# Optimization experiments

Measured on AMD Instinct MI355X. Metric: run time of the kernel, lower is better.

## Reference

```python
import jax, jax.numpy as jnp
import numpy as np

BATCH = 1024
INPUT_DIM = 4096
HIDDEN_DIM = 4096
N_BLOCKS = 8
BLOCK_SIZE = HIDDEN_DIM // N_BLOCKS          # 512
IN_BLOCK_SIZE = INPUT_DIM // N_BLOCKS        # 512


def setup_inputs() -> dict:
    key = jax.random.key(0)
    ks = jax.random.split(key, 6)
    scale = 1.0 / np.sqrt(BLOCK_SIZE)  # torch GRUCell init: U(-1/sqrt(hidden), 1/sqrt(hidden))
    return {
        "x": jax.random.normal(ks[0], (BATCH, INPUT_DIM), dtype=jnp.float32),
        "h": jax.random.normal(ks[1], (BATCH, HIDDEN_DIM), dtype=jnp.float32),
        "W_ih": jax.random.normal(ks[2], (N_BLOCKS, 3 * BLOCK_SIZE, IN_BLOCK_SIZE), dtype=jnp.float32) * scale,
        "W_hh": jax.random.normal(ks[3], (N_BLOCKS, 3 * BLOCK_SIZE, BLOCK_SIZE), dtype=jnp.float32) * scale,
        "b_ih": jax.random.normal(ks[4], (N_BLOCKS, 3 * BLOCK_SIZE), dtype=jnp.float32) * scale,
        "b_hh": jax.random.normal(ks[5], (N_BLOCKS, 3 * BLOCK_SIZE), dtype=jnp.float32) * scale,
    }


def reference(x, h, W_ih, W_hh, b_ih, b_hh):
    B = x.shape[0]
    n, g3, ibs = W_ih.shape           # n_blocks, 3*block_size, input_block_size
    bs = W_hh.shape[2]                # block_size
    xb = x.reshape(B, n, ibs)         # (B, n_blocks, input_block_size)
    hb = h.reshape(B, n, bs)          # (B, n_blocks, block_size)
    # Block-diagonal GEMM: one grouped matmul over all blocks at once.
    gi = jnp.einsum('bni,ngi->bng', xb, W_ih) + b_ih   # (B, n, 3*bs)
    gh = jnp.einsum('bnh,ngh->bng', hb, W_hh) + b_hh   # (B, n, 3*bs)
    i_r, i_z, i_n = jnp.split(gi, 3, axis=-1)
    h_r, h_z, h_n = jnp.split(gh, 3, axis=-1)
    r = jax.nn.sigmoid(i_r + h_r)                      # reset gate
    z = jax.nn.sigmoid(i_z + h_z)                      # update gate
    n_gate = jnp.tanh(i_n + r * h_n)                   # candidate state
    new_h = n_gate + z * (hb - n_gate)                 # torch GRUCell: h' = (1-z)*n + z*h
    return new_h.reshape(B, n * bs)
```

## Files before the change

### kernel.cpp

```cpp
#include <hip/hip_runtime.h>
#include <hip/hip_bf16.h>
#include <stdint.h>

#define G1CAST(p) ((const __attribute__((address_space(1))) void*)(p))
#define L3CAST(p) ((__attribute__((address_space(3))) void*)(p))

typedef short bf16x8 __attribute__((ext_vector_type(8)));
typedef float f32x16 __attribute__((ext_vector_type(16)));

static __device__ __forceinline__ short f2bf(float f) {
    __hip_bfloat16 b = __float2bfloat16(f);
    return __builtin_bit_cast(short, b);
}

__global__ __launch_bounds__(256) void wconv_kernel(const float* __restrict__ Wih,
                                                    const float* __restrict__ Whh,
                                                    short* __restrict__ Wstep) {
    const int b = blockIdx.x;
    const int vb = (b & 7) * 768 + (b >> 3);
    const int gid = vb * 256 + threadIdx.x;
    const int lane = gid & 63;
    int t1 = gid >> 6;
    const int g = t1 % 3;  t1 /= 3;
    const int wn = t1 & 1; t1 >>= 1;
    const int s = t1 & 63; t1 >>= 6;
    const int jt = t1 & 7;
    const int nblk = t1 >> 3;
    const int j = jt * 64 + wn * 32 + (lane & 31);
    const int kk = s * 16 + (lane >> 5) * 8;
    const float* src = (kk < 512)
        ? Wih + ((int64_t)nblk * 786432 + (int64_t)(g * 512 + j) * 512 + kk)
        : Whh + ((int64_t)nblk * 786432 + (int64_t)(g * 512 + j) * 512 + (kk - 512));
    const float4 a = ((const float4*)src)[0];
    const float4 bq = ((const float4*)src)[1];
    bf16x8 o;
    o[0] = f2bf(a.x); o[1] = f2bf(a.y); o[2] = f2bf(a.z); o[3] = f2bf(a.w);
    o[4] = f2bf(bq.x); o[5] = f2bf(bq.y); o[6] = f2bf(bq.z); o[7] = f2bf(bq.w);
    *(bf16x8*)(Wstep + (size_t)gid * 8) = o;
}

__global__ __launch_bounds__(256) void aconv_kernel(const float* __restrict__ x,
                                                    const float* __restrict__ h,
                                                    short* __restrict__ Afrag) {
    const int b = blockIdx.x;
    const int n = b & 7;
    const int inner = b >> 3;
    const int rb = inner >> 4;
    const int u = inner & 15;
    const int tid = threadIdx.x;
    const int lane = tid & 63;
    const int s = u * 4 + (tid >> 6);
    const int row = rb * 32 + (lane & 31);
    const int kk = s * 16 + (lane >> 5) * 8;
    const float* src = (kk < 512)
        ? x + ((size_t)row * 4096 + n * 512 + kk)
        : h + ((size_t)row * 4096 + n * 512 + (kk - 512));
    const float4 a = ((const float4*)src)[0];
    const float4 bq = ((const float4*)src)[1];
    bf16x8 o;
    o[0] = f2bf(a.x); o[1] = f2bf(a.y); o[2] = f2bf(a.z); o[3] = f2bf(a.w);
    o[4] = f2bf(bq.x); o[5] = f2bf(bq.y); o[6] = f2bf(bq.z); o[7] = f2bf(bq.w);
    const size_t dst = ((((size_t)(rb * 8 + n) * 64 + s) * 64) + lane) * 8;
    *(bf16x8*)(Afrag + dst) = o;
}

__global__ __launch_bounds__(256, 2) void gru_kernel(
    const float* __restrict__ hst,
    const short* __restrict__ Wstep, const short* __restrict__ Afrag,
    const float* __restrict__ b_ih, const float* __restrict__ b_hh,
    float* __restrict__ out)
{
    __shared__ char ldsB[6][8192];

    const int tid = threadIdx.x;
    const int nblk = blockIdx.x & 7;
    const int rr_ = blockIdx.x >> 3;
    const int bt = rr_ >> 3;
    const int jt = rr_ & 7;
    const int brow0 = bt * 128;

    const int lane = tid & 63;
    const int wave = tid >> 6;
    const int wm = wave >> 1;
    const int wn = wave & 1;
    const int l31 = lane & 31;
    const int k8 = lane >> 5;

    const int rb0 = (brow0 + wm * 64) >> 5;
    const char* ab0 = (const char*)Afrag + ((size_t)(rb0 * 8 + nblk) << 16) + (size_t)lane * 16;
    const char* ab1 = ab0 + (8 << 16);

    const int d0 = wave * 2048;
    const int ssrc0 = (d0 >= 6144) ? d0 - 6144 : d0;
    const int ssrc1 = (d0 + 1024 >= 6144) ? d0 + 1024 - 6144 : d0 + 1024;
    const char* wstep0 = (const char*)Wstep + (size_t)((nblk * 8 + jt) * 64) * 6144
                       + (size_t)lane * 16;
    const int boff = (wn * 3) * 1024 + lane * 16;

    f32x16 acc_r[2] = {};
    f32x16 acc_z[2] = {};
    f32x16 acc_nx[2] = {};
    f32x16 acc_nh[2] = {};

    bf16x8 a0P, a1P, a0Q, a1Q, a0R, a1R, a0S, a1S;

#define LDA(T, s_v)                                                        \
    {                                                                      \
        const int sc = (s_v) > 63 ? 63 : (s_v);                            \
        a0##T = *(const bf16x8*)(ab0 + (size_t)sc * 1024);                 \
        a1##T = *(const bf16x8*)(ab1 + (size_t)sc * 1024);                 \
    }

    auto stageB = [&](int s, int slot) {
        const int sc = s > 63 ? 63 : s;
        const char* src = wstep0 + (size_t)sc * 6144;
        char* dst = (char*)&ldsB[slot][0] + d0;
        __builtin_amdgcn_global_load_lds(G1CAST(src + ssrc0), L3CAST(dst), 16, 0, 0);
        __builtin_amdgcn_global_load_lds(G1CAST(src + ssrc1), L3CAST(dst + 1024), 16, 0, 0);
    };

#define ITER(C, L, accN)                                                            \
    {                                                                               \
        __builtin_amdgcn_s_barrier();                                               \
        __builtin_amdgcn_sched_barrier(0);                                          \
        stageB(s_ + 5, wslot);                                                      \
        LDA(L, s_ + 3)                                                              \
        __builtin_amdgcn_sched_barrier(0);                                          \
        asm volatile("s_waitcnt vmcnt(12)" ::: "memory");                           \
        __builtin_amdgcn_sched_barrier(0);                                          \
        const char* bp = &ldsB[rslot][boff];                                        \
        bf16x8 b0 = *(const bf16x8*)(bp);                                           \
        bf16x8 b1 = *(const bf16x8*)(bp + 1024);                                    \
        bf16x8 b2 = *(const bf16x8*)(bp + 2048);                                    \
        __builtin_amdgcn_s_setprio(1);                                              \
        acc_r[0] = __builtin_amdgcn_mfma_f32_32x32x16_bf16(a0##C, b0, acc_r[0], 0, 0, 0); \
        acc_r[1] = __builtin_amdgcn_mfma_f32_32x32x16_bf16(a1##C, b0, acc_r[1], 0, 0, 0); \
        acc_z[0] = __builtin_amdgcn_mfma_f32_32x32x16_bf16(a0##C, b1, acc_z[0], 0, 0, 0); \
        acc_z[1] = __builtin_amdgcn_mfma_f32_32x32x16_bf16(a1##C, b1, acc_z[1], 0, 0, 0); \
        accN[0]  = __builtin_amdgcn_mfma_f32_32x32x16_bf16(a0##C, b2, accN[0], 0, 0, 0);  \
        accN[1]  = __builtin_amdgcn_mfma_f32_32x32x16_bf16(a1##C, b2, accN[1], 0, 0, 0);  \
        __builtin_amdgcn_s_setprio(0);                                              \
        rslot = (rslot == 5) ? 0 : rslot + 1;                                       \
        wslot = (wslot == 5) ? 0 : wslot + 1;                                       \
        s_ += 1;                                                                    \
    }

    stageB(0, 0); stageB(1, 1); stageB(2, 2); stageB(3, 3); stageB(4, 4);
    LDA(P, 0) LDA(Q, 1) LDA(R, 2)
    __builtin_amdgcn_sched_barrier(0);
    asm volatile("s_waitcnt vmcnt(12)" ::: "memory");
    __builtin_amdgcn_sched_barrier(0);

    int s_ = 0;
    int rslot = 0;
    int wslot = 5;

    #pragma unroll 1
    for (int g4 = 0; g4 < 8; ++g4) {
        ITER(P, S, acc_nx)
        ITER(Q, P, acc_nx)
        ITER(R, Q, acc_nx)
        ITER(S, R, acc_nx)
    }
    #pragma unroll 1
    for (int g4 = 0; g4 < 8; ++g4) {
        ITER(P, S, acc_nh)
        ITER(Q, P, acc_nh)
        ITER(R, Q, acc_nh)
        ITER(S, R, acc_nh)
    }
#undef ITER
#undef LDA

    const int jb = jt * 64 + wn * 32 + l31;
    const int bb = nblk * 1536 + jb;
    const float br = b_ih[bb] + b_hh[bb];
    const float bz = b_ih[bb + 512] + b_hh[bb + 512];
    const float bnx = b_ih[bb + 1024];
    const float bnh = b_hh[bb + 1024];
    const int gcol = nblk * 512 + jb;
    #pragma unroll
    for (int m = 0; m < 2; ++m) {
        #pragma unroll
        for (int rr = 0; rr < 16; ++rr) {
            const int rowl = (rr & 3) + 8 * (rr >> 2) + 4 * k8;
            const int row = brow0 + wm * 64 + m * 32 + rowl;
            const size_t idx = (size_t)row * 4096 + gcol;
            const float sr = acc_r[m][rr] + br;
            const float sz = acc_z[m][rr] + bz;
            const float rg = 1.f / (1.f + __expf(-sr));
            const float zg = 1.f / (1.f + __expf(-sz));
            const float tin = (acc_nx[m][rr] + bnx) + rg * (acc_nh[m][rr] + bnh);
            const float e2 = __expf(-2.f * tin);
            const float ng = 2.f / (1.f + e2) - 1.f;
            const float hv = hst[idx];
            out[idx] = ng + zg * (hv - ng);
        }
    }
}

extern "C" void kernel_launch(void* const* d_in, const int* in_sizes, int n_in,
                              void* d_out, int out_size, void* d_ws, size_t ws_size,
                              hipStream_t stream) {
    (void)in_sizes; (void)n_in; (void)out_size; (void)ws_size;
    const float* x    = (const float*)d_in[0];
    const float* h    = (const float*)d_in[1];
    const float* W_ih = (const float*)d_in[2];
    const float* W_hh = (const float*)d_in[3];
    const float* b_ih = (const float*)d_in[4];
    const float* b_hh = (const float*)d_in[5];
    short* Wstep = (short*)d_ws;
    short* Afrag = (short*)d_ws + (size_t)12 * 1024 * 1024;

    wconv_kernel<<<6144, 256, 0, stream>>>(W_ih, W_hh, Wstep);
    aconv_kernel<<<4096, 256, 0, stream>>>(x, h, Afrag);
    gru_kernel<<<512, 256, 0, stream>>>(h, Wstep, Afrag, b_ih, b_hh, (float*)d_out);
}
```

Baseline: 60.32 us.

## Stage activation fragments through LDS via async global-to-LDS loads

Activation (A) fragments were previously loaded straight from global memory into registers by every wave, with a four-register rotation, so the two waves sharing a row tile fetched identical data. Now each wave issues one async global_load_lds per step into a 6-slot LDS ring next to the weight tiles, and both column waves read A from LDS. This cuts duplicate A traffic from global memory and frees the A prefetch registers. In exchange it adds LDS reads and LDS footprint per block. The unchanged vmcnt(12) now waits deeper into the prefetch queue, which shortens the effective lookahead.

```diff
diff --git a/kernel.cpp b/kernel.cpp
--- a/kernel.cpp
+++ b/kernel.cpp
@@ -70,7 +70,8 @@
     const float* __restrict__ b_ih, const float* __restrict__ b_hh,
     float* __restrict__ out)
 {
-    __shared__ char ldsB[6][8192];
+    __shared__ __align__(16) char ldsB[6][8192];
+    __shared__ __align__(16) char ldsA[6][4096];
 
     const int tid = threadIdx.x;
     const int nblk = blockIdx.x & 7;
@@ -86,70 +87,59 @@
     const int l31 = lane & 31;
     const int k8 = lane >> 5;
 
-    const int rb0 = (brow0 + wm * 64) >> 5;
-    const char* ab0 = (const char*)Afrag + ((size_t)(rb0 * 8 + nblk) << 16) + (size_t)lane * 16;
-    const char* ab1 = ab0 + (8 << 16);
-
     const int d0 = wave * 2048;
     const int ssrc0 = (d0 >= 6144) ? d0 - 6144 : d0;
     const int ssrc1 = (d0 + 1024 >= 6144) ? d0 + 1024 - 6144 : d0 + 1024;
     const char* wstep0 = (const char*)Wstep + (size_t)((nblk * 8 + jt) * 64) * 6144
                        + (size_t)lane * 16;
+    const char* asrc0 = (const char*)Afrag
+        + ((size_t)(((brow0 >> 5) + wave) * 8 + nblk) << 16) + (size_t)lane * 16;
+
     const int boff = (wn * 3) * 1024 + lane * 16;
+    const int aoff = wm * 2048 + lane * 16;
 
     f32x16 acc_r[2] = {};
     f32x16 acc_z[2] = {};
     f32x16 acc_nx[2] = {};
     f32x16 acc_nh[2] = {};
 
-    bf16x8 a0P, a1P, a0Q, a1Q, a0R, a1R, a0S, a1S;
-
-#define LDA(T, s_v)                                                        \
-    {                                                                      \
-        const int sc = (s_v) > 63 ? 63 : (s_v);                            \
-        a0##T = *(const bf16x8*)(ab0 + (size_t)sc * 1024);                 \
-        a1##T = *(const bf16x8*)(ab1 + (size_t)sc * 1024);                 \
-    }
-
-    auto stageB = [&](int s, int slot) {
+    auto stageAB = [&](int s, int slot) {
         const int sc = s > 63 ? 63 : s;
-        const char* src = wstep0 + (size_t)sc * 6144;
-        char* dst = (char*)&ldsB[slot][0] + d0;
-        __builtin_amdgcn_global_load_lds(G1CAST(src + ssrc0), L3CAST(dst), 16, 0, 0);
-        __builtin_amdgcn_global_load_lds(G1CAST(src + ssrc1), L3CAST(dst + 1024), 16, 0, 0);
+        const char* bsrc = wstep0 + (size_t)sc * 6144;
+        char* bdst = (char*)&ldsB[slot][0] + d0;
+        __builtin_amdgcn_global_load_lds(G1CAST(bsrc + ssrc0), L3CAST(bdst), 16, 0, 0);
+        __builtin_amdgcn_global_load_lds(G1CAST(bsrc + ssrc1), L3CAST(bdst + 1024), 16, 0, 0);
+        __builtin_amdgcn_global_load_lds(G1CAST(asrc0 + (size_t)sc * 1024),
+                                         L3CAST((char*)&ldsA[slot][0] + wave * 1024), 16, 0, 0);
     };
 
-#define ITER(C, L, accN)                                                            \
+#define ITER(accN)                                                                  \
     {                                                                               \
         __builtin_amdgcn_s_barrier();                                               \
-        __builtin_amdgcn_sched_barrier(0);                                          \
-        stageB(s_ + 5, wslot);                                                      \
-        LDA(L, s_ + 3)                                                              \
+        stageAB(s_ + 5, wslot);                                                     \
         __builtin_amdgcn_sched_barrier(0);                                          \
         asm volatile("s_waitcnt vmcnt(12)" ::: "memory");                           \
-        __builtin_amdgcn_sched_barrier(0);                                          \
         const char* bp = &ldsB[rslot][boff];                                        \
+        const char* ap = &ldsA[rslot][aoff];                                        \
+        bf16x8 a0v = *(const bf16x8*)(ap);                                          \
+        bf16x8 a1v = *(const bf16x8*)(ap + 1024);                                   \
         bf16x8 b0 = *(const bf16x8*)(bp);                                           \
         bf16x8 b1 = *(const bf16x8*)(bp + 1024);                                    \
         bf16x8 b2 = *(const bf16x8*)(bp + 2048);                                    \
         __builtin_amdgcn_s_setprio(1);                                              \
-        acc_r[0] = __builtin_amdgcn_mfma_f32_32x32x16_bf16(a0##C, b0, acc_r[0], 0, 0, 0); \
-        acc_r[1] = __builtin_amdgcn_mfma_f32_32x32x16_bf16(a1##C, b0, acc_r[1], 0, 0, 0); \
-        acc_z[0] = __builtin_amdgcn_mfma_f32_32x32x16_bf16(a0##C, b1, acc_z[0], 0, 0, 0); \
-        acc_z[1] = __builtin_amdgcn_mfma_f32_32x32x16_bf16(a1##C, b1, acc_z[1], 0, 0, 0); \
-        accN[0]  = __builtin_amdgcn_mfma_f32_32x32x16_bf16(a0##C, b2, accN[0], 0, 0, 0);  \
-        accN[1]  = __builtin_amdgcn_mfma_f32_32x32x16_bf16(a1##C, b2, accN[1], 0, 0, 0);  \
+        acc_r[0] = __builtin_amdgcn_mfma_f32_32x32x16_bf16(a0v, b0, acc_r[0], 0, 0, 0); \
+        acc_r[1] = __builtin_amdgcn_mfma_f32_32x32x16_bf16(a1v, b0, acc_r[1], 0, 0, 0); \
+        acc_z[0] = __builtin_amdgcn_mfma_f32_32x32x16_bf16(a0v, b1, acc_z[0], 0, 0, 0); \
+        acc_z[1] = __builtin_amdgcn_mfma_f32_32x32x16_bf16(a1v, b1, acc_z[1], 0, 0, 0); \
+        accN[0]  = __builtin_amdgcn_mfma_f32_32x32x16_bf16(a0v, b2, accN[0], 0, 0, 0);  \
+        accN[1]  = __builtin_amdgcn_mfma_f32_32x32x16_bf16(a1v, b2, accN[1], 0, 0, 0);  \
         __builtin_amdgcn_s_setprio(0);                                              \
         rslot = (rslot == 5) ? 0 : rslot + 1;                                       \
         wslot = (wslot == 5) ? 0 : wslot + 1;                                       \
         s_ += 1;                                                                    \
     }
 
-    stageB(0, 0); stageB(1, 1); stageB(2, 2); stageB(3, 3); stageB(4, 4);
-    LDA(P, 0) LDA(Q, 1) LDA(R, 2)
-    __builtin_amdgcn_sched_barrier(0);
-    asm volatile("s_waitcnt vmcnt(12)" ::: "memory");
-    __builtin_amdgcn_sched_barrier(0);
+    stageAB(0, 0); stageAB(1, 1); stageAB(2, 2); stageAB(3, 3); stageAB(4, 4);
 
     int s_ = 0;
     int rslot = 0;
@@ -157,20 +147,13 @@
 
     #pragma unroll 1
     for (int g4 = 0; g4 < 8; ++g4) {
-        ITER(P, S, acc_nx)
-        ITER(Q, P, acc_nx)
-        ITER(R, Q, acc_nx)
-        ITER(S, R, acc_nx)
+        ITER(acc_nx) ITER(acc_nx) ITER(acc_nx) ITER(acc_nx)
     }
     #pragma unroll 1
     for (int g4 = 0; g4 < 8; ++g4) {
-        ITER(P, S, acc_nh)
-        ITER(Q, P, acc_nh)
-        ITER(R, Q, acc_nh)
-        ITER(S, R, acc_nh)
+        ITER(acc_nh) ITER(acc_nh) ITER(acc_nh) ITER(acc_nh)
     }
 #undef ITER
-#undef LDA
 
     const int jb = jt * 64 + wn * 32 + l31;
     const int bb = nblk * 1536 + jb;
```

Measured after the change: 70.72 us. 1.17x slower.

## Halve GRU block row tile and raise occupancy with shallower LDS pipeline

Applied to the files above, without the earlier changes.

The GRU GEMM block tile shrinks from 128 to 64 batch rows, so each wave computes one 32-row MFMA tile instead of two, and the grid doubles to 1024 blocks. Launch bounds now allow 4 blocks per SM, and the LDS weight ring drops from 6 to 4 slots with a prefetch distance of 3 instead of 5. The aim is more resident waves to hide memory latency and a better-balanced grid across CUs. The cost is that each staged weight tile is reused by half as many rows, which doubles weight traffic, and the shallower prefetch has less slack.

```diff
diff --git a/kernel.cpp b/kernel.cpp
--- a/kernel.cpp
+++ b/kernel.cpp
@@ -64,20 +64,20 @@
     *(bf16x8*)(Afrag + dst) = o;
 }
 
-__global__ __launch_bounds__(256, 2) void gru_kernel(
+__global__ __launch_bounds__(256, 4) void gru_kernel(
     const float* __restrict__ hst,
     const short* __restrict__ Wstep, const short* __restrict__ Afrag,
     const float* __restrict__ b_ih, const float* __restrict__ b_hh,
     float* __restrict__ out)
 {
-    __shared__ char ldsB[6][8192];
+    __shared__ __align__(16) char ldsB[4][8192];
 
     const int tid = threadIdx.x;
     const int nblk = blockIdx.x & 7;
     const int rr_ = blockIdx.x >> 3;
+    const int jt = rr_ & 7;
     const int bt = rr_ >> 3;
-    const int jt = rr_ & 7;
-    const int brow0 = bt * 128;
+    const int brow0 = bt * 64;
 
     const int lane = tid & 63;
     const int wave = tid >> 6;
@@ -86,29 +86,26 @@
     const int l31 = lane & 31;
     const int k8 = lane >> 5;
 
-    const int rb0 = (brow0 + wm * 64) >> 5;
-    const char* ab0 = (const char*)Afrag + ((size_t)(rb0 * 8 + nblk) << 16) + (size_t)lane * 16;
-    const char* ab1 = ab0 + (8 << 16);
-
     const int d0 = wave * 2048;
     const int ssrc0 = (d0 >= 6144) ? d0 - 6144 : d0;
     const int ssrc1 = (d0 + 1024 >= 6144) ? d0 + 1024 - 6144 : d0 + 1024;
     const char* wstep0 = (const char*)Wstep + (size_t)((nblk * 8 + jt) * 64) * 6144
                        + (size_t)lane * 16;
+    const char* ab = (const char*)Afrag
+        + ((size_t)((bt * 2 + wm) * 8 + nblk) << 16) + (size_t)lane * 16;
     const int boff = (wn * 3) * 1024 + lane * 16;
 
-    f32x16 acc_r[2] = {};
-    f32x16 acc_z[2] = {};
-    f32x16 acc_nx[2] = {};
-    f32x16 acc_nh[2] = {};
-
-    bf16x8 a0P, a1P, a0Q, a1Q, a0R, a1R, a0S, a1S;
+    f32x16 acc_r = {};
+    f32x16 acc_z = {};
+    f32x16 acc_nx = {};
+    f32x16 acc_nh = {};
+
+    bf16x8 aP, aQ, aR, aS;
 
 #define LDA(T, s_v)                                                        \
     {                                                                      \
         const int sc = (s_v) > 63 ? 63 : (s_v);                            \
-        a0##T = *(const bf16x8*)(ab0 + (size_t)sc * 1024);                 \
-        a1##T = *(const bf16x8*)(ab1 + (size_t)sc * 1024);                 \
+        a##T = *(const bf16x8*)(ab + (size_t)sc * 1024);                   \
     }
 
     auto stageB = [&](int s, int slot) {
@@ -122,38 +119,26 @@
 #define ITER(C, L, accN)                                                            \
     {                                                                               \
         __builtin_amdgcn_s_barrier();                                               \
-        __builtin_amdgcn_sched_barrier(0);                                          \
-        stageB(s_ + 5, wslot);                                                      \
+        stageB(s_ + 3, (s_ + 3) & 3);                                               \
         LDA(L, s_ + 3)                                                              \
         __builtin_amdgcn_sched_barrier(0);                                          \
-        asm volatile("s_waitcnt vmcnt(12)" ::: "memory");                           \
-        __builtin_amdgcn_sched_barrier(0);                                          \
-        const char* bp = &ldsB[rslot][boff];                                        \
+        asm volatile("s_waitcnt vmcnt(6)" ::: "memory");                            \
+        const char* bp = &ldsB[s_ & 3][boff];                                       \
         bf16x8 b0 = *(const bf16x8*)(bp);                                           \
         bf16x8 b1 = *(const bf16x8*)(bp + 1024);                                    \
         bf16x8 b2 = *(const bf16x8*)(bp + 2048);                                    \
         __builtin_amdgcn_s_setprio(1);                                              \
-        acc_r[0] = __builtin_amdgcn_mfma_f32_32x32x16_bf16(a0##C, b0, acc_r[0], 0, 0, 0); \
-        acc_r[1] = __builtin_amdgcn_mfma_f32_32x32x16_bf16(a1##C, b0, acc_r[1], 0, 0, 0); \
-        acc_z[0] = __builtin_amdgcn_mfma_f32_32x32x16_bf16(a0##C, b1, acc_z[0], 0, 0, 0); \
-        acc_z[1] = __builtin_amdgcn_mfma_f32_32x32x16_bf16(a1##C, b1, acc_z[1], 0, 0, 0); \
-        accN[0]  = __builtin_amdgcn_mfma_f32_32x32x16_bf16(a0##C, b2, accN[0], 0, 0, 0);  \
-        accN[1]  = __builtin_amdgcn_mfma_f32_32x32x16_bf16(a1##C, b2, accN[1], 0, 0, 0);  \
+        acc_r = __builtin_amdgcn_mfma_f32_32x32x16_bf16(a##C, b0, acc_r, 0, 0, 0);  \
+        acc_z = __builtin_amdgcn_mfma_f32_32x32x16_bf16(a##C, b1, acc_z, 0, 0, 0);  \
+        accN  = __builtin_amdgcn_mfma_f32_32x32x16_bf16(a##C, b2, accN, 0, 0, 0);   \
         __builtin_amdgcn_s_setprio(0);                                              \
-        rslot = (rslot == 5) ? 0 : rslot + 1;                                       \
-        wslot = (wslot == 5) ? 0 : wslot + 1;                                       \
         s_ += 1;                                                                    \
     }
 
-    stageB(0, 0); stageB(1, 1); stageB(2, 2); stageB(3, 3); stageB(4, 4);
+    stageB(0, 0); stageB(1, 1); stageB(2, 2);
     LDA(P, 0) LDA(Q, 1) LDA(R, 2)
-    __builtin_amdgcn_sched_barrier(0);
-    asm volatile("s_waitcnt vmcnt(12)" ::: "memory");
-    __builtin_amdgcn_sched_barrier(0);
 
     int s_ = 0;
-    int rslot = 0;
-    int wslot = 5;
 
     #pragma unroll 1
     for (int g4 = 0; g4 < 8; ++g4) {
@@ -180,22 +165,19 @@
     const float bnh = b_hh[bb + 1024];
     const int gcol = nblk * 512 + jb;
     #pragma unroll
-    for (int m = 0; m < 2; ++m) {
-        #pragma unroll
-        for (int rr = 0; rr < 16; ++rr) {
-            const int rowl = (rr & 3) + 8 * (rr >> 2) + 4 * k8;
-            const int row = brow0 + wm * 64 + m * 32 + rowl;
-            const size_t idx = (size_t)row * 4096 + gcol;
-            const float sr = acc_r[m][rr] + br;
-            const float sz = acc_z[m][rr] + bz;
-            const float rg = 1.f / (1.f + __expf(-sr));
-            const float zg = 1.f / (1.f + __expf(-sz));
-            const float tin = (acc_nx[m][rr] + bnx) + rg * (acc_nh[m][rr] + bnh);
-            const float e2 = __expf(-2.f * tin);
-            const float ng = 2.f / (1.f + e2) - 1.f;
-            const float hv = hst[idx];
-            out[idx] = ng + zg * (hv - ng);
-        }
+    for (int rr = 0; rr < 16; ++rr) {
+        const int rowl = (rr & 3) + 8 * (rr >> 2) + 4 * k8;
+        const int row = brow0 + wm * 32 + rowl;
+        const size_t idx = (size_t)row * 4096 + gcol;
+        const float sr = acc_r[rr] + br;
+        const float sz = acc_z[rr] + bz;
+        const float rg = 1.f / (1.f + __expf(-sr));
+        const float zg = 1.f / (1.f + __expf(-sz));
+        const float tin = (acc_nx[rr] + bnx) + rg * (acc_nh[rr] + bnh);
+        const float e2 = __expf(-2.f * tin);
+        const float ng = 2.f / (1.f + e2) - 1.f;
+        const float hv = hst[idx];
+        out[idx] = ng + zg * (hv - ng);
     }
 }
 
@@ -214,5 +196,5 @@
 
     wconv_kernel<<<6144, 256, 0, stream>>>(W_ih, W_hh, Wstep);
     aconv_kernel<<<4096, 256, 0, stream>>>(x, h, Afrag);
-    gru_kernel<<<512, 256, 0, stream>>>(h, Wstep, Afrag, b_ih, b_hh, (float*)d_out);
-}
+    gru_kernel<<<1024, 256, 0, stream>>>(h, Wstep, Afrag, b_ih, b_hh, (float*)d_out);
+}
```

Measured after the change: 63.75 us. +5.7%, slower.
